# Kernel tuning notes

Hardware: AMD Instinct MI355X
Metric: run time of the kernel (lower is better)

Reference implementation:

```python
import jax, jax.numpy as jnp
import numpy as np

CONTEXT = 3  # config['context']
B, H, W = 8, 256, 256
NBR = 2 * CONTEXT  # number of similarity branches


def _conv(x, w, b):
    # x: [N, Cin, H, W], w: [Cout, Cin, kh, kw], SAME padding, stride 1
    y = jax.lax.conv_general_dilated(x, w, (1, 1), 'SAME',
                                     dimension_numbers=('NCHW', 'OIHW', 'NCHW'))
    return y + b[None, :, None, None]


def setup_inputs() -> dict:
    key = jax.random.key(0)
    ks = jax.random.split(key, 5)
    x = jax.random.normal(ks[0], (B, 2 * CONTEXT + 1, H, W), dtype=jnp.float32)
    # kaiming-ish scaled inits
    W1 = jax.random.normal(ks[1], (NBR, 64, 2, 3, 3), dtype=jnp.float32) * (2.0 / (64 * 9)) ** 0.5
    b1 = jnp.zeros((NBR, 64), dtype=jnp.float32)
    W2 = jax.random.normal(ks[2], (NBR, 1, 64, 1, 1), dtype=jnp.float32) * (2.0 / 1) ** 0.5 * 0.1
    b2 = jnp.zeros((NBR, 1), dtype=jnp.float32)
    Wm = jax.random.normal(ks[3], (7, 7, 3, 3), dtype=jnp.float32) * (2.0 / (7 * 9)) ** 0.5
    bm = jnp.zeros((7,), dtype=jnp.float32)
    return {'x': x, 'W1': W1, 'b1': b1, 'W2': W2, 'b2': b2, 'Wm': Wm, 'bm': bm}


def reference(x, W1, b1, W2, b2, Wm, bm):
    # mode == 'context' path just returns x; this implements the main path.
    base = x[:, CONTEXT:CONTEXT + 1]                                  # [B,1,H,W]
    checks = jnp.concatenate([x[:, :CONTEXT], x[:, CONTEXT + 1:]], axis=1)  # [B,6,H,W]
    check_e = checks[:, :, None]                                      # [B,6,1,H,W]
    base_e = jnp.broadcast_to(base[:, None], check_e.shape)           # [B,6,1,H,W]
    # channel order: pre-frames -> (base, check); post-frames -> (check, base)
    ch0 = jnp.concatenate([base_e[:, :CONTEXT], check_e[:, CONTEXT:]], axis=2 - 2 + 2)  # placeholder
    ch0 = jnp.concatenate([base_e[:, :CONTEXT], check_e[:, CONTEXT:]], axis=1)
    ch1 = jnp.concatenate([check_e[:, :CONTEXT], base_e[:, CONTEXT:]], axis=1)
    pairs = jnp.concatenate([ch0, ch1], axis=2)                       # [B,6,2,H,W]
    pairs = jnp.swapaxes(pairs, 0, 1)                                 # [6,B,2,H,W]

    def branch(pair, w1, bb1, w2, bb2):
        h = jax.nn.relu(_conv(pair, w1, bb1))                         # [B,64,H,W]
        return jax.nn.sigmoid(_conv(h, w2, bb2))                      # [B,1,H,W]

    sims = jax.vmap(branch)(pairs, W1, b1, W2, b2)                    # [6,B,1,H,W]
    weighted = sims[:, :, 0] * jnp.swapaxes(checks, 0, 1)             # [6,B,H,W]
    weighted = jnp.swapaxes(weighted, 0, 1)                           # [B,6,H,W]
    combined = jnp.concatenate([weighted[:, :CONTEXT], base, weighted[:, CONTEXT:]], axis=1)  # [B,7,H,W]
    return _conv(combined, Wm, bm)                                    # [B,7,H,W]
```

## Files before the change

### kernel.cpp

```cpp
#include <hip/hip_runtime.h>
#include <math.h>

#define Bn 8
#define Hn 256
#define Wn 256
#define HW (Hn * Wn)
#define ROWS 4
#define RPL 6
#define RP 264
#define ZW (12 * RP)

typedef __attribute__((ext_vector_type(8))) short bf16x8;
typedef __attribute__((ext_vector_type(4))) float f32x4;
typedef __attribute__((ext_vector_type(2))) float f32x2;

__device__ __forceinline__ unsigned int pk_bits(unsigned int lo,
                                                unsigned int hi) {
  return __builtin_amdgcn_perm(hi, lo, 0x07060302u);
}
__device__ __forceinline__ unsigned int pk_bf16(float lo, float hi) {
  return pk_bits(__float_as_uint(lo), __float_as_uint(hi));
}
__device__ __forceinline__ f32x2 fma2(float s, f32x2 a, f32x2 c) {
  f32x2 sv = {s, s};
  return sv * a + c;
}


__global__ __launch_bounds__(256, 4) void sim_kernel(
    const float* __restrict__ x,
    const float* __restrict__ W1,
    const float* __restrict__ b1,
    const float* __restrict__ W2,
    const float* __restrict__ b2,
    float* __restrict__ comb)
{
  __shared__ float rowsF[12 * RP + 64];
  __shared__ uint4 wq[4][64];

  int bi = blockIdx.x;
  int n  = bi >> 9;
  int b  = (bi >> 6) & 7;
  int h0 = (bi & 63) * ROWS;
  int cc = (n < 3) ? n : n + 1;
  int t = threadIdx.x;

  const float* xb     = x + (size_t)b * 7 * HW;
  const float* basep  = xb + 3 * HW;
  const float* checkp = xb + (size_t)cc * HW;

  {
    int f = t >> 6, qq = (t >> 4) & 3, m = t & 15;
    int bsrc = (n < 3) ? 0 : 1;
    const float* wch = W1 + ((size_t)(n * 64 + 16 * f + m)) * 18;
    int g0pl = (qq == 2) ? 1 : 0;
    int g0dx = (qq == 0) ? 0 : (qq == 1) ? 2 : 1;
    int g1pl = (qq == 0) ? 0 : 1;
    int g1dx = (qq == 0) ? 1 : (qq == 1) ? 0 : 2;
    float wg0[3], wg1[3];
#pragma unroll
    for (int rrs = 0; rrs < 3; ++rrs) {
      wg0[rrs] = (qq <= 2)
          ? wch[(g0pl ? 1 - bsrc : bsrc) * 9 + rrs * 3 + g0dx] : 0.f;
      wg1[rrs] = (qq <= 2)
          ? wch[(g1pl ? 1 - bsrc : bsrc) * 9 + rrs * 3 + g1dx] : 0.f;
    }
    unsigned int kv[4];
    kv[0] = pk_bf16(wg0[0], wg0[1]);
    kv[1] = pk_bf16(wg0[2], 0.f);
    kv[2] = pk_bf16(wg1[0], wg1[1]);
    kv[3] = pk_bf16(wg1[2], 0.f);
    wq[f][(qq << 4) + m] = make_uint4(kv[0], kv[1], kv[2], kv[3]);
  }

  int lane = t & 63, wvid = t >> 6;
  int q = lane >> 4, m_ = lane & 15;
  f32x2 w2A[4], w2B[4];
  f32x4 b1vv[4];
#pragma unroll
  for (int f = 0; f < 4; ++f) {
    float4 tw = *(const float4*)&W2[n * 64 + 16 * f + 4 * q];
    float4 tb = *(const float4*)&b1[n * 64 + 16 * f + 4 * q];
    w2A[f][0] = tw.x; w2A[f][1] = tw.y;
    w2B[f][0] = tw.z; w2B[f][1] = tw.w;
    b1vv[f][0] = tb.x; b1vv[f][1] = tb.y;
    b1vv[f][2] = tb.z; b1vv[f][3] = tb.w;
  }
  float bbl = b2[n] * -1.442695041f;

  {
    int col = (t & 63) << 2;
#pragma unroll
    for (int it = 0; it < 3; ++it) {
      int rf = it * 4 + (t >> 6);
      int pl = (rf >= RPL) ? 1 : 0;
      int j  = rf - pl * RPL;
      int hh = h0 - 1 + j;
      const float* src = pl ? checkp : basep;
      float4 val = make_float4(0.f, 0.f, 0.f, 0.f);
      if ((unsigned)hh < (unsigned)Hn)
        val = *(const float4*)(src + hh * Wn + col);
      *(float4*)&rowsF[rf * RP + 4 + col] = val;
    }
    if (t < 12) {
      rowsF[t * RP + 3] = 0.f;
      rowsF[t * RP + 260] = 0.f;
    }
    if (t >= 192) rowsF[ZW + (t - 192)] = 0.f;
  }

  const unsigned int* rowsU = (const unsigned int*)rowsF;
  int g0pl = (q == 2) ? 1 : 0;
  int g0dx = (q == 0) ? 0 : (q == 1) ? 2 : 1;
  int g1pl = (q == 0) ? 0 : 1;
  int g1dx = (q == 0) ? 1 : (q == 1) ? 0 : 2;
  unsigned int addrG0, addrG1, step;
  if (q <= 2) {
    addrG0 = (unsigned)((g0pl * RPL) * RP + 3 + g0dx + wvid * 64 + m_);
    addrG1 = (unsigned)((g1pl * RPL) * RP + 3 + g1dx + wvid * 64 + m_);
    step = (unsigned)RP;
  } else {
    addrG0 = (unsigned)ZW;
    addrG1 = (unsigned)ZW;
    step = 0u;
  }
  int bpaddr = ((lane ^ 32) << 2);

  __syncthreads();

  bf16x8 afrag[4];
#pragma unroll
  for (int f = 0; f < 4; ++f) afrag[f] = *(const bf16x8*)&wq[f][lane];

  float* combcc = comb + ((size_t)b * 7 + cc) * HW;
  int pxs = wvid * 64 + lane;
  bool bb1 = (lane & 32) != 0;
  bool bb0 = (lane & 16) != 0;

  unsigned int va[3][4], vb[3][4];
#pragma unroll
  for (int s = 0; s < 4; s += 2) {
    va[0][s]     = rowsU[addrG0 + s * 16];
    va[0][s + 1] = rowsU[addrG0 + s * 16 + 16];
    vb[0][s]     = rowsU[addrG1 + s * 16];
    vb[0][s + 1] = rowsU[addrG1 + s * 16 + 16];
  }
  addrG0 += step; addrG1 += step;
#pragma unroll
  for (int s = 0; s < 4; s += 2) {
    va[1][s]     = rowsU[addrG0 + s * 16];
    va[1][s + 1] = rowsU[addrG0 + s * 16 + 16];
    vb[1][s]     = rowsU[addrG1 + s * 16];
    vb[1][s + 1] = rowsU[addrG1 + s * 16 + 16];
  }
  addrG0 += step; addrG1 += step;

#pragma unroll 1
  for (int r = 0; r < ROWS; ++r) {
    float ccv = rowsF[(RPL + r + 1) * RP + 4 + pxs];

#pragma unroll
    for (int s = 0; s < 4; s += 2) {
      va[2][s]     = rowsU[addrG0 + s * 16];
      va[2][s + 1] = rowsU[addrG0 + s * 16 + 16];
      vb[2][s]     = rowsU[addrG1 + s * 16];
      vb[2][s + 1] = rowsU[addrG1 + s * 16 + 16];
    }
    addrG0 += step; addrG1 += step;

    float P[4];
#pragma unroll
    for (int sp = 0; sp < 2; ++sp) {
      int s0 = 2 * sp, s1 = 2 * sp + 1;
      union { unsigned int u[4]; bf16x8 v; } u0, u1;
      u0.u[0] = pk_bits(va[0][s0], va[1][s0]);
      u0.u[1] = pk_bits(va[2][s0], va[2][s0]);
      u0.u[2] = pk_bits(vb[0][s0], vb[1][s0]);
      u0.u[3] = pk_bits(vb[2][s0], vb[2][s0]);
      u1.u[0] = pk_bits(va[0][s1], va[1][s1]);
      u1.u[1] = pk_bits(va[2][s1], va[2][s1]);
      u1.u[2] = pk_bits(vb[0][s1], vb[1][s1]);
      u1.u[3] = pk_bits(vb[2][s1], vb[2][s1]);

      f32x4 acc0[4], acc1[4];
#pragma unroll
      for (int f = 0; f < 4; ++f) {
        acc0[f] = __builtin_amdgcn_mfma_f32_16x16x32_bf16(afrag[f], u0.v,
                                                          b1vv[f], 0, 0, 0);
        acc1[f] = __builtin_amdgcn_mfma_f32_16x16x32_bf16(afrag[f], u1.v,
                                                          b1vv[f], 0, 0, 0);
      }
      f32x2 sA0 = {0.f, 0.f}, sB0 = {0.f, 0.f};
      f32x2 sA1 = {0.f, 0.f}, sB1 = {0.f, 0.f};
#pragma unroll
      for (int f = 0; f < 4; ++f) {
        f32x2 a01, a23, c01, c23;
        a01[0] = acc0[f][0]; a01[1] = acc0[f][1];
        a23[0] = acc0[f][2]; a23[1] = acc0[f][3];
        c01[0] = acc1[f][0]; c01[1] = acc1[f][1];
        c23[0] = acc1[f][2]; c23[1] = acc1[f][3];
        a01 = __builtin_elementwise_max(a01, (f32x2)0.f);
        a23 = __builtin_elementwise_max(a23, (f32x2)0.f);
        c01 = __builtin_elementwise_max(c01, (f32x2)0.f);
        c23 = __builtin_elementwise_max(c23, (f32x2)0.f);
        sA0 += w2A[f] * a01;
        sB0 += w2B[f] * a23;
        sA1 += w2A[f] * c01;
        sB1 += w2B[f] * c23;
      }
      f32x2 s0v = sA0 + sB0, s1v = sA1 + sB1;
      P[s0] = s0v[0] + s0v[1];
      P[s1] = s1v[0] + s1v[1];
    }

    float U0 = bb1 ? P[0] : P[2];
    float U1 = bb1 ? P[1] : P[3];
    float r0 = __int_as_float(
        __builtin_amdgcn_ds_bpermute(bpaddr, __float_as_int(U0)));
    float r1 = __int_as_float(
        __builtin_amdgcn_ds_bpermute(bpaddr, __float_as_int(U1)));
    float T0 = (bb1 ? P[2] : P[0]) + r0;
    float T1 = (bb1 ? P[3] : P[1]) + r1;
    float Wv = bb0 ? T0 : T1;
    float r2 = __int_as_float(
        __builtin_amdgcn_ds_swizzle(__float_as_int(Wv), 0x401F));
    float S = (bb0 ? T1 : T0) + r2;

    float e = __builtin_amdgcn_exp2f(fmaf(S, -1.442695041f, bbl));
    float g = __builtin_amdgcn_rcpf(1.f + e);
    combcc[(h0 + r) * Wn + pxs] = g * ccv;

#pragma unroll
    for (int s = 0; s < 4; ++s) {
      va[0][s] = va[1][s]; va[1][s] = va[2][s];
      vb[0][s] = vb[1][s]; vb[1][s] = vb[2][s];
    }
  }
}

__global__ __launch_bounds__(512) void mix_kernel(
    const float* __restrict__ comb,
    const float* __restrict__ x,
    const float* __restrict__ Wm,
    const float* __restrict__ bm,
    float* __restrict__ out)
{
  __shared__ float mr[42 * RP];

  int bi = blockIdx.x;
  int b  = bi >> 6;
  int h0 = (bi & 63) << 2;
  int t = threadIdx.x;

  for (int u = t; u < 42 * 64; u += 512) {
    int rf = u >> 6;
    int col = (u & 63) << 2;
    int ic = rf / 6, j = rf - ic * 6;
    int hh = h0 - 1 + j;
    const float* src = (ic == 3) ? (x + ((size_t)b * 7 + 3) * HW)
                                 : (comb + ((size_t)b * 7 + ic) * HW);
    float4 v = make_float4(0.f, 0.f, 0.f, 0.f);
    if ((unsigned)hh < (unsigned)Hn)
      v = *(const float4*)(src + hh * Wn + col);
    *(float4*)&mr[rf * RP + 4 + col] = v;
  }
  if (t < 42) {
    mr[t * RP + 3] = 0.f;
    mr[t * RP + 260] = 0.f;
  }
  __syncthreads();

  int r   = t >> 7;
  int px0 = (t & 127) << 1;
  int h   = h0 + r;

  f32x2 acc[7];
#pragma unroll
  for (int oc = 0; oc < 7; ++oc) {
    float bv = bm[oc];
    acc[oc] = (f32x2){bv, bv};
  }

#pragma unroll 1
  for (int ic = 0; ic < 7; ++ic) {
    f32x2 PP[3][3];
#pragma unroll
    for (int dy = 0; dy < 3; ++dy) {
      const float* rp = &mr[(ic * 6 + r + dy) * RP + 3 + px0];
      float v0 = rp[0], v1 = rp[1], v2 = rp[2], v3 = rp[3];
      PP[dy][0] = (f32x2){v0, v1};
      PP[dy][1] = (f32x2){v1, v2};
      PP[dy][2] = (f32x2){v2, v3};
    }
    const float* wp = Wm + ic * 9;
#pragma unroll
    for (int oc = 0; oc < 7; ++oc) {
      const float* wo = wp + oc * 63;
#pragma unroll
      for (int dy = 0; dy < 3; ++dy) {
        float w0 = wo[dy * 3], w1 = wo[dy * 3 + 1], w2 = wo[dy * 3 + 2];
        acc[oc] = fma2(w0, PP[dy][0],
                   fma2(w1, PP[dy][1], fma2(w2, PP[dy][2], acc[oc])));
      }
    }
  }

  float* ob = out + (size_t)b * 7 * HW + h * Wn + px0;
#pragma unroll
  for (int oc = 0; oc < 7; ++oc)
    *(float2*)(ob + (size_t)oc * HW) = make_float2(acc[oc][0], acc[oc][1]);
}

extern "C" void kernel_launch(void* const* d_in, const int* in_sizes, int n_in,
                              void* d_out, int out_size, void* d_ws, size_t ws_size,
                              hipStream_t stream) {
  const float* x  = (const float*)d_in[0];
  const float* W1 = (const float*)d_in[1];
  const float* b1 = (const float*)d_in[2];
  const float* W2 = (const float*)d_in[3];
  const float* b2 = (const float*)d_in[4];
  const float* Wm = (const float*)d_in[5];
  const float* bm = (const float*)d_in[6];
  float* out  = (float*)d_out;
  float* comb = (float*)d_ws;

  sim_kernel<<<6 * 8 * (Hn / ROWS), 256, 0, stream>>>(x, W1, b1, W2, b2, comb);
  mix_kernel<<<8 * (Hn / 4), 512, 0, stream>>>(comb, x, Wm, bm, out);
}
```

Baseline: 112.8 us.

## Pre-pack adjacent-row bf16 pairs in shared memory and fully unroll row loop

The staging step now loads two consecutive input rows per slot and stores them already packed as bf16 pairs, so the inner loop reads ready-made MFMA operand words instead of packing per row with perm instructions. All six packed row slots are preloaded into registers and the row loop is fully unrolled, removing the rolling register shifts. The center check value is read from global memory instead of LDS, and occupancy hint drops from 4 to 3 blocks per CU to allow more registers. This doubles global loads during staging and raises register pressure in exchange for fewer per-row LDS reads and pack ops.

```diff
diff --git a/kernel.cpp b/kernel.cpp
--- a/kernel.cpp
+++ b/kernel.cpp
@@ -8,6 +8,7 @@
 #define ROWS 4
 #define RPL 6
 #define RP 264
+#define PO (RPL*RP)
 #define ZW (12 * RP)
 
 typedef __attribute__((ext_vector_type(8))) short bf16x8;
@@ -27,7 +28,7 @@
 }
 
 
-__global__ __launch_bounds__(256, 4) void sim_kernel(
+__global__ __launch_bounds__(256, 3) void sim_kernel(
     const float* __restrict__ x,
     const float* __restrict__ W1,
     const float* __restrict__ b1,
@@ -35,7 +36,7 @@
     const float* __restrict__ b2,
     float* __restrict__ comb)
 {
-  __shared__ float rowsF[12 * RP + 64];
+  __shared__ unsigned int pairU[12 * RP + 64];
   __shared__ uint4 wq[4][64];
 
   int bi = blockIdx.x;
@@ -95,34 +96,41 @@
       int rf = it * 4 + (t >> 6);
       int pl = (rf >= RPL) ? 1 : 0;
       int j  = rf - pl * RPL;
-      int hh = h0 - 1 + j;
       const float* src = pl ? checkp : basep;
-      float4 val = make_float4(0.f, 0.f, 0.f, 0.f);
-      if ((unsigned)hh < (unsigned)Hn)
-        val = *(const float4*)(src + hh * Wn + col);
-      *(float4*)&rowsF[rf * RP + 4 + col] = val;
+      int hlo = h0 - 1 + j, hhi = h0 + j;
+      float4 vlo = make_float4(0.f, 0.f, 0.f, 0.f);
+      float4 vhi = make_float4(0.f, 0.f, 0.f, 0.f);
+      if ((unsigned)hlo < (unsigned)Hn)
+        vlo = *(const float4*)(src + hlo * Wn + col);
+      if ((unsigned)hhi < (unsigned)Hn)
+        vhi = *(const float4*)(src + hhi * Wn + col);
+      uint4 pk;
+      pk.x = pk_bf16(vlo.x, vhi.x);
+      pk.y = pk_bf16(vlo.y, vhi.y);
+      pk.z = pk_bf16(vlo.z, vhi.z);
+      pk.w = pk_bf16(vlo.w, vhi.w);
+      *(uint4*)&pairU[rf * RP + 4 + col] = pk;
     }
     if (t < 12) {
-      rowsF[t * RP + 3] = 0.f;
-      rowsF[t * RP + 260] = 0.f;
-    }
-    if (t >= 192) rowsF[ZW + (t - 192)] = 0.f;
-  }
-
-  const unsigned int* rowsU = (const unsigned int*)rowsF;
+      pairU[t * RP + 3] = 0u;
+      pairU[t * RP + 260] = 0u;
+    }
+    if (t >= 192) pairU[ZW + (t - 192)] = 0u;
+  }
+
   int g0pl = (q == 2) ? 1 : 0;
   int g0dx = (q == 0) ? 0 : (q == 1) ? 2 : 1;
   int g1pl = (q == 0) ? 0 : 1;
   int g1dx = (q == 0) ? 1 : (q == 1) ? 0 : 2;
-  unsigned int addrG0, addrG1, step;
+  unsigned int aG0, aG1, stepv;
   if (q <= 2) {
-    addrG0 = (unsigned)((g0pl * RPL) * RP + 3 + g0dx + wvid * 64 + m_);
-    addrG1 = (unsigned)((g1pl * RPL) * RP + 3 + g1dx + wvid * 64 + m_);
-    step = (unsigned)RP;
+    aG0 = (unsigned)(g0pl * PO + 3 + g0dx + wvid * 64 + m_);
+    aG1 = (unsigned)(g1pl * PO + 3 + g1dx + wvid * 64 + m_);
+    stepv = (unsigned)RP;
   } else {
-    addrG0 = (unsigned)ZW;
-    addrG1 = (unsigned)ZW;
-    step = 0u;
+    aG0 = (unsigned)ZW;
+    aG1 = (unsigned)ZW;
+    stepv = 0u;
   }
   int bpaddr = ((lane ^ 32) << 2);
 
@@ -137,50 +145,30 @@
   bool bb1 = (lane & 32) != 0;
   bool bb0 = (lane & 16) != 0;
 
-  unsigned int va[3][4], vb[3][4];
-#pragma unroll
-  for (int s = 0; s < 4; s += 2) {
-    va[0][s]     = rowsU[addrG0 + s * 16];
-    va[0][s + 1] = rowsU[addrG0 + s * 16 + 16];
-    vb[0][s]     = rowsU[addrG1 + s * 16];
-    vb[0][s + 1] = rowsU[addrG1 + s * 16 + 16];
-  }
-  addrG0 += step; addrG1 += step;
-#pragma unroll
-  for (int s = 0; s < 4; s += 2) {
-    va[1][s]     = rowsU[addrG0 + s * 16];
-    va[1][s + 1] = rowsU[addrG0 + s * 16 + 16];
-    vb[1][s]     = rowsU[addrG1 + s * 16];
-    vb[1][s + 1] = rowsU[addrG1 + s * 16 + 16];
-  }
-  addrG0 += step; addrG1 += step;
-
-#pragma unroll 1
+  unsigned int Pj[6][2][4];
+#pragma unroll
+  for (int j = 0; j < 6; ++j) {
+    unsigned int a0 = aG0 + j * stepv, a1 = aG1 + j * stepv;
+#pragma unroll
+    for (int s = 0; s < 4; ++s) {
+      Pj[j][0][s] = pairU[a0 + s * 16];
+      Pj[j][1][s] = pairU[a1 + s * 16];
+    }
+  }
+
+#pragma unroll
   for (int r = 0; r < ROWS; ++r) {
-    float ccv = rowsF[(RPL + r + 1) * RP + 4 + pxs];
-
-#pragma unroll
-    for (int s = 0; s < 4; s += 2) {
-      va[2][s]     = rowsU[addrG0 + s * 16];
-      va[2][s + 1] = rowsU[addrG0 + s * 16 + 16];
-      vb[2][s]     = rowsU[addrG1 + s * 16];
-      vb[2][s + 1] = rowsU[addrG1 + s * 16 + 16];
-    }
-    addrG0 += step; addrG1 += step;
+    float ccv = checkp[(h0 + r) * Wn + pxs];
 
     float P[4];
 #pragma unroll
     for (int sp = 0; sp < 2; ++sp) {
-      int s0 = 2 * sp, s1 = 2 * sp + 1;
+      int s0 = 2 * sp, s1 = s0 + 1;
       union { unsigned int u[4]; bf16x8 v; } u0, u1;
-      u0.u[0] = pk_bits(va[0][s0], va[1][s0]);
-      u0.u[1] = pk_bits(va[2][s0], va[2][s0]);
-      u0.u[2] = pk_bits(vb[0][s0], vb[1][s0]);
-      u0.u[3] = pk_bits(vb[2][s0], vb[2][s0]);
-      u1.u[0] = pk_bits(va[0][s1], va[1][s1]);
-      u1.u[1] = pk_bits(va[2][s1], va[2][s1]);
-      u1.u[2] = pk_bits(vb[0][s1], vb[1][s1]);
-      u1.u[3] = pk_bits(vb[2][s1], vb[2][s1]);
+      u0.u[0] = Pj[r][0][s0];     u0.u[1] = Pj[r + 2][0][s0];
+      u0.u[2] = Pj[r][1][s0];     u0.u[3] = Pj[r + 2][1][s0];
+      u1.u[0] = Pj[r][0][s1];     u1.u[1] = Pj[r + 2][0][s1];
+      u1.u[2] = Pj[r][1][s1];     u1.u[3] = Pj[r + 2][1][s1];
 
       f32x4 acc0[4], acc1[4];
 #pragma unroll
@@ -229,12 +217,6 @@
     float e = __builtin_amdgcn_exp2f(fmaf(S, -1.442695041f, bbl));
     float g = __builtin_amdgcn_rcpf(1.f + e);
     combcc[(h0 + r) * Wn + pxs] = g * ccv;
-
-#pragma unroll
-    for (int s = 0; s < 4; ++s) {
-      va[0][s] = va[1][s]; va[1][s] = va[2][s];
-      vb[0][s] = vb[1][s]; vb[1][s] = vb[2][s];
-    }
   }
 }
 
```

After: 110.7 us. About the same (-1.8%).
